# Optimization experiments

Hardware: AMD Instinct MI355X
Metric: run time of the kernel (lower is better)

## Reference

```python
import jax, jax.numpy as jnp
import numpy as np

D_MODEL, N_HEADS, D_FF = 768, 12, 3072
B, S = 2, 2048
EPS = 1e-6

def _ln(x, alpha, bias):
    # Matches torch: std with Bessel correction (unbiased), scalar alpha/bias
    mean = x.mean(axis=-1, keepdims=True)
    std = jnp.std(x, axis=-1, keepdims=True, ddof=1)
    return alpha * (x - mean) / (std + EPS) + bias

def setup_inputs() -> dict:
    key = jax.random.key(0)
    ks = jax.random.split(key, 12)
    def w(k, shp):
        return jax.random.normal(k, shp, dtype=jnp.float32) * 0.02
    inp = {
        "x": jax.random.normal(ks[0], (B, S, D_MODEL), dtype=jnp.float32),
        "mask": jnp.ones((B, 1, 1, S), dtype=jnp.int32),
        "wq": w(ks[1], (D_MODEL, D_MODEL)), "bq": jnp.zeros((D_MODEL,), jnp.float32),
        "wk": w(ks[2], (D_MODEL, D_MODEL)), "bk": jnp.zeros((D_MODEL,), jnp.float32),
        "wv": w(ks[3], (D_MODEL, D_MODEL)), "bv": jnp.zeros((D_MODEL,), jnp.float32),
        "wo": w(ks[4], (D_MODEL, D_MODEL)), "bo": jnp.zeros((D_MODEL,), jnp.float32),
        "w1": w(ks[5], (D_MODEL, D_FF)), "b1": jnp.zeros((D_FF,), jnp.float32),
        "w2": w(ks[6], (D_FF, D_MODEL)), "b2": jnp.zeros((D_MODEL,), jnp.float32),
        "ln1_a": jnp.ones((1,), jnp.float32), "ln1_b": jnp.zeros((1,), jnp.float32),
        "ln2_a": jnp.ones((1,), jnp.float32), "ln2_b": jnp.zeros((1,), jnp.float32),
    }
    return inp

def reference(x, mask, wq, bq, wk, bk, wv, bv, wo, bo, w1, b1, w2, b2,
              ln1_a, ln1_b, ln2_a, ln2_b):
    d_k = D_MODEL // N_HEADS
    # --- residual 1: pre-LN self-attention ---
    h = _ln(x, ln1_a, ln1_b)
    q = (h @ wq + bq).reshape(B, S, N_HEADS, d_k).transpose(0, 2, 1, 3)
    k = (h @ wk + bk).reshape(B, S, N_HEADS, d_k).transpose(0, 2, 1, 3)
    v = (h @ wv + bv).reshape(B, S, N_HEADS, d_k).transpose(0, 2, 1, 3)
    scores = jnp.einsum('bhqd,bhkd->bhqk', q, k) / jnp.sqrt(jnp.float32(d_k))
    scores = jnp.where(mask == 0, jnp.float32(-1e9), scores)
    attn = jax.nn.softmax(scores, axis=-1)            # [B,H,S,S] materialized, as in source
    ctx = jnp.einsum('bhqk,bhkd->bhqd', attn, v)
    ctx = ctx.transpose(0, 2, 1, 3).reshape(B, S, D_MODEL)
    x = x + (ctx @ wo + bo)
    # --- residual 2: pre-LN FFN ---
    h = _ln(x, ln2_a, ln2_b)
    ffn = jax.nn.relu(h @ w1 + b1) @ w2 + b2
    return x + ffn
```

## Files before the change

### kernel.cpp

```cpp
#include <hip/hip_runtime.h>
#include <math.h>

#define DM    768
#define NH    12
#define DKH   64
#define DFF   3072
#define BATCH 2
#define SLEN  2048
#define MTOT  4096
#define LNEPS 1e-6f
#define QSCALE 0.18033688011112042f

typedef unsigned short u16;
typedef __attribute__((ext_vector_type(8))) short bf16x8;
typedef __attribute__((ext_vector_type(4))) float f32x4;
typedef __attribute__((ext_vector_type(4))) unsigned short us4;

__device__ __forceinline__ u16 f2bf(float f) {
    union { float f; unsigned int u; } v; v.f = f;
    unsigned int r = v.u + 0x7FFFu + ((v.u >> 16) & 1u);
    return (u16)(r >> 16);
}

__device__ __forceinline__ unsigned pk2bf_t(float lo, float hi) {
    union { float f; unsigned u; } a, b;
    a.f = lo; b.f = hi;
    return __builtin_amdgcn_perm(b.u, a.u, 0x07060302u);
}

__device__ __forceinline__ void gld16(const void* g, void* lds) {
    __builtin_amdgcn_global_load_lds(
        (const __attribute__((address_space(1))) unsigned int*)(unsigned long long)g,
        (__attribute__((address_space(3))) unsigned int*)(unsigned int)(unsigned long long)lds,
        16, 0, 0);
}

__device__ __forceinline__ void xcd_map(int id, int Nb, int& bm, int& bn) {
    int xcd = id & 7, loc = id >> 3;
    bn = loc % Nb;
    bm = (loc / Nb) * 8 + xcd;
}

__device__ __forceinline__ void ln_body(const float* __restrict__ x,
                                        u16* __restrict__ out,
                                        const float* __restrict__ alpha_p,
                                        const float* __restrict__ beta_p,
                                        const float* __restrict__ b2,
                                        float* __restrict__ out2, int row) {
    const float* xr = x + (size_t)row * DM;
    int t = threadIdx.x;
    float v0 = xr[t], v1 = xr[t + 256], v2 = xr[t + 512];
    float s = v0 + v1 + v2;
    #pragma unroll
    for (int off = 32; off > 0; off >>= 1) s += __shfl_down(s, off);
    __shared__ float red[4], red2[4];
    int wv = t >> 6, ln = t & 63;
    if (ln == 0) red[wv] = s;
    __syncthreads();
    float mean = (red[0] + red[1] + red[2] + red[3]) * (1.0f / 768.0f);
    float d0 = v0 - mean, d1 = v1 - mean, d2 = v2 - mean;
    float sq = d0 * d0 + d1 * d1 + d2 * d2;
    #pragma unroll
    for (int off = 32; off > 0; off >>= 1) sq += __shfl_down(sq, off);
    if (ln == 0) red2[wv] = sq;
    __syncthreads();
    float var = (red2[0] + red2[1] + red2[2] + red2[3]) * (1.0f / 767.0f);
    float scale = alpha_p[0] / (sqrtf(var) + LNEPS);
    float bias = beta_p[0];
    u16* orow = out + (size_t)row * DM;
    orow[t]       = f2bf(d0 * scale + bias);
    orow[t + 256] = f2bf(d1 * scale + bias);
    orow[t + 512] = f2bf(d2 * scale + bias);
    if (out2) {
        float* o2 = out2 + (size_t)row * DM;
        o2[t]       = v0 + b2[t];
        o2[t + 256] = v1 + b2[t + 256];
        o2[t + 512] = v2 + b2[t + 512];
    }
}

__global__ __launch_bounds__(256) void ln_kernel(const float* __restrict__ x,
                                                 u16* __restrict__ out,
                                                 const float* __restrict__ alpha_p,
                                                 const float* __restrict__ beta_p,
                                                 const float* __restrict__ b2,
                                                 float* __restrict__ out2) {
    ln_body(x, out, alpha_p, beta_p, b2, out2, blockIdx.x);
}

__device__ __forceinline__ void wcast_body(const float* __restrict__ src,
                                           u16* __restrict__ dst,
                                           int R, int C, int bx, int by) {
    __shared__ float tile[32][33];
    int t = threadIdx.x, tx = t & 31, ty = t >> 5;
    int r0 = by * 32, c0 = bx * 32;
    #pragma unroll
    for (int p = 0; p < 4; p++)
        tile[ty + p * 8][tx] = src[(size_t)(r0 + ty + p * 8) * C + c0 + tx];
    __syncthreads();
    #pragma unroll
    for (int p = 0; p < 4; p++)
        dst[(size_t)(c0 + ty + p * 8) * R + r0 + tx] = f2bf(tile[tx][ty + p * 8]);
}

__global__ __launch_bounds__(256) void prep_kernel(
        const float* __restrict__ x, u16* __restrict__ h,
        const float* __restrict__ ln1a, const float* __restrict__ ln1b,
        const float* __restrict__ wq, const float* __restrict__ wk,
        const float* __restrict__ wv, const float* __restrict__ wo,
        const float* __restrict__ w1, const float* __restrict__ w2,
        u16* __restrict__ wqT, u16* __restrict__ wkT, u16* __restrict__ wvT,
        u16* __restrict__ woT, u16* __restrict__ w1T, u16* __restrict__ w2T) {
    int bid = blockIdx.x;
    if (bid < MTOT) {
        ln_body(x, h, ln1a, ln1b, nullptr, nullptr, bid);
        return;
    }
    bid -= MTOT;
    const float* src; u16* dst; int R, C, bx, by;
    if (bid < 2304) {
        int j = bid / 576, tix = bid % 576;
        R = 768; C = 768; bx = tix % 24; by = tix / 24;
        src = (j == 0) ? wq : (j == 1) ? wk : (j == 2) ? wv : wo;
        dst = (j == 0) ? wqT : (j == 1) ? wkT : (j == 2) ? wvT : woT;
    } else if (bid < 4608) {
        int tix = bid - 2304;
        R = 768; C = 3072; bx = tix % 96; by = tix / 96;
        src = w1; dst = w1T;
    } else {
        int tix = bid - 4608;
        R = 3072; C = 768; bx = tix % 24; by = tix / 24;
        src = w2; dst = w2T;
    }
    wcast_body(src, dst, R, C, bx, by);
}

template<int EPI>
__device__ __forceinline__ void gemm128_core(const u16* __restrict__ A,
                                             const u16* __restrict__ Wt,
                                             const float* __restrict__ bias,
                                             const float* __restrict__ resid,
                                             void* __restrict__ Cout,
                                             int M, int N, int Kstride, int Kloop,
                                             float scale, int bm, int bn) {
    __shared__ __align__(16) u16 As[2][128 * 32];
    __shared__ __align__(16) u16 Bs[2][128 * 32];
    int t = threadIdx.x;
    int ln = t & 63, w = t >> 6;
    int wm = w >> 1, wn = w & 1;
    int quad = ln >> 4, col = ln & 15;
    int m0 = bm * 128, n0 = bn * 128;

    f32x4 acc[4][4];
    const f32x4 zero = {0.f, 0.f, 0.f, 0.f};
    #pragma unroll
    for (int i = 0; i < 4; i++)
        #pragma unroll
        for (int j = 0; j < 4; j++) acc[i][j] = zero;

    int st_ch = (((ln & 3) ^ ((ln >> 3) & 3))) * 8;
    const u16* Ag = A  + (size_t)(m0 + 32 * w + (ln >> 2)) * Kstride + st_ch;
    const u16* Bg = Wt + (size_t)(n0 + 32 * w + (ln >> 2)) * Kstride + st_ch;

    gld16(Ag,                As[0] + w * 1024);
    gld16(Ag + 16 * Kstride, As[0] + w * 1024 + 512);
    gld16(Bg,                Bs[0] + w * 1024);
    gld16(Bg + 16 * Kstride, Bs[0] + w * 1024 + 512);
    __syncthreads();

    int rch = (quad ^ ((col >> 1) & 3)) * 8;

    for (int k0 = 0; k0 < Kloop; k0 += 32) {
        int cur = (k0 >> 5) & 1, nxt = cur ^ 1;
        if (k0 + 32 < Kloop) {
            gld16(Ag + k0 + 32,                As[nxt] + w * 1024);
            gld16(Ag + k0 + 32 + 16 * Kstride, As[nxt] + w * 1024 + 512);
            gld16(Bg + k0 + 32,                Bs[nxt] + w * 1024);
            gld16(Bg + k0 + 32 + 16 * Kstride, Bs[nxt] + w * 1024 + 512);
        }
        bf16x8 af[4], bfr[4];
        #pragma unroll
        for (int i = 0; i < 4; i++)
            af[i] = *(const bf16x8*)&As[cur][(wm * 64 + i * 16 + col) * 32 + rch];
        #pragma unroll
        for (int j = 0; j < 4; j++)
            bfr[j] = *(const bf16x8*)&Bs[cur][(wn * 64 + j * 16 + col) * 32 + rch];
        #pragma unroll
        for (int i = 0; i < 4; i++)
            #pragma unroll
            for (int j = 0; j < 4; j++)
                acc[i][j] = __builtin_amdgcn_mfma_f32_16x16x32_bf16(af[i], bfr[j], acc[i][j], 0, 0, 0);
        __syncthreads();
    }

    #pragma unroll
    for (int i = 0; i < 4; i++) {
        int mb = m0 + wm * 64 + i * 16 + quad * 4;
        #pragma unroll
        for (int j = 0; j < 4; j++) {
            int n = n0 + wn * 64 + j * 16 + col;
            if (EPI == 0 || EPI == 1) {
                float bs = bias[n];
                u16* Cb = (u16*)Cout;
                #pragma unroll
                for (int r = 0; r < 4; r++) {
                    float f = (acc[i][j][r] + bs) * ((EPI == 0) ? scale : 1.0f);
                    if (EPI == 1) f = fmaxf(f, 0.f);
                    Cb[(size_t)(mb + r) * N + n] = f2bf(f);
                }
            } else if (EPI == 2) {
                float bs = bias[n];
                float* Cf = (float*)Cout;
                #pragma unroll
                for (int r = 0; r < 4; r++)
                    Cf[(size_t)(mb + r) * N + n] =
                        acc[i][j][r] + bs + resid[(size_t)(mb + r) * N + n];
            } else if (EPI == 3) {
                float bs = bias[n];
                u16* Cb = (u16*)Cout;
                us4 pk;
                #pragma unroll
                for (int r = 0; r < 4; r++) pk[r] = f2bf(acc[i][j][r] + bs);
                *(us4*)&Cb[(size_t)n * M + mb] = pk;
            } else {
                float* Cf = (float*)Cout;
                #pragma unroll
                for (int r = 0; r < 4; r++)
                    atomicAdd(&Cf[(size_t)(mb + r) * N + n], acc[i][j][r]);
            }
        }
    }
}

template<int EPI>
__global__ __launch_bounds__(256) void gemm_kernel(const u16* __restrict__ A,
                                                   const u16* __restrict__ Wt,
                                                   const float* __restrict__ bias,
                                                   const float* __restrict__ resid,
                                                   void* __restrict__ C,
                                                   int M, int N, int Kstride, int Kloop,
                                                   float scale, int Nb) {
    const u16* Az = A  + (size_t)blockIdx.z * Kloop;
    const u16* Wz = Wt + (size_t)blockIdx.z * Kloop;
    int bm, bn;
    xcd_map(blockIdx.x, Nb, bm, bn);
    gemm128_core<EPI>(Az, Wz, bias, resid, C, M, N, Kstride, Kloop, scale, bm, bn);
}

__global__ __launch_bounds__(256) void qkv_kernel(const u16* __restrict__ h,
        const u16* __restrict__ wqT, const u16* __restrict__ wkT, const u16* __restrict__ wvT,
        const float* __restrict__ bq, const float* __restrict__ bk, const float* __restrict__ bv,
        u16* __restrict__ q, u16* __restrict__ k, u16* __restrict__ vT) {
    int z = blockIdx.z;
    int bm, bn;
    xcd_map(blockIdx.x, 6, bm, bn);
    if (z == 0)      gemm128_core<0>(h, wqT, bq, nullptr, q,  MTOT, DM, DM, DM, QSCALE, bm, bn);
    else if (z == 1) gemm128_core<0>(h, wkT, bk, nullptr, k,  MTOT, DM, DM, DM, 1.0f,   bm, bn);
    else             gemm128_core<3>(h, wvT, bv, nullptr, vT, MTOT, DM, DM, DM, 1.0f,   bm, bn);
}

template<int EPI>
__global__ __launch_bounds__(256) void gemm64_kernel(const u16* __restrict__ A,
                                                     const u16* __restrict__ Wt,
                                                     const float* __restrict__ bias,
                                                     const float* __restrict__ resid,
                                                     void* __restrict__ Cout,
                                                     int M, int N, int Kstride, int Kloop,
                                                     int Nb) {
    __shared__ __align__(16) u16 As[2][64 * 32];
    __shared__ __align__(16) u16 Bs[2][64 * 32];
    int t = threadIdx.x, ln = t & 63, w = t >> 6;
    int wm = w >> 1, wn = w & 1;
    int quad = ln >> 4, col = ln & 15;
    int bm, bn;
    xcd_map(blockIdx.x, Nb, bm, bn);
    int m0 = bm * 64, n0 = bn * 64;

    f32x4 acc[2][2];
    const f32x4 zero = {0.f, 0.f, 0.f, 0.f};
    #pragma unroll
    for (int i = 0; i < 2; i++)
        #pragma unroll
        for (int j = 0; j < 2; j++) acc[i][j] = zero;

    int st_ch = (((ln & 3) ^ ((ln >> 3) & 3))) * 8;
    const u16* Ag = A  + (size_t)(m0 + 16 * w + (ln >> 2)) * Kstride + st_ch;
    const u16* Bg = Wt + (size_t)(n0 + 16 * w + (ln >> 2)) * Kstride + st_ch;
    gld16(Ag, As[0] + w * 512);
    gld16(Bg, Bs[0] + w * 512);
    __syncthreads();

    int rch = (quad ^ ((col >> 1) & 3)) * 8;

    for (int k0 = 0; k0 < Kloop; k0 += 32) {
        int cur = (k0 >> 5) & 1, nxt = cur ^ 1;
        if (k0 + 32 < Kloop) {
            gld16(Ag + k0 + 32, As[nxt] + w * 512);
            gld16(Bg + k0 + 32, Bs[nxt] + w * 512);
        }
        bf16x8 af[2], bfr[2];
        #pragma unroll
        for (int i = 0; i < 2; i++)
            af[i] = *(const bf16x8*)&As[cur][(wm * 32 + i * 16 + col) * 32 + rch];
        #pragma unroll
        for (int j = 0; j < 2; j++)
            bfr[j] = *(const bf16x8*)&Bs[cur][(wn * 32 + j * 16 + col) * 32 + rch];
        #pragma unroll
        for (int i = 0; i < 2; i++)
            #pragma unroll
            for (int j = 0; j < 2; j++)
                acc[i][j] = __builtin_amdgcn_mfma_f32_16x16x32_bf16(af[i], bfr[j], acc[i][j], 0, 0, 0);
        __syncthreads();
    }

    #pragma unroll
    for (int i = 0; i < 2; i++) {
        int mb = m0 + wm * 32 + i * 16 + quad * 4;
        #pragma unroll
        for (int j = 0; j < 2; j++) {
            int n = n0 + wn * 32 + j * 16 + col;
            float bs = bias[n];
            float* Cf = (float*)Cout;
            #pragma unroll
            for (int r = 0; r < 4; r++)
                Cf[(size_t)(mb + r) * N + n] =
                    acc[i][j][r] + bs + resid[(size_t)(mb + r) * N + n];
        }
    }
}

__global__ __launch_bounds__(256) void attn_kernel(const u16* __restrict__ qg,
                                                   const u16* __restrict__ kg,
                                                   const u16* __restrict__ vTg,
                                                   const int* __restrict__ mask,
                                                   u16* __restrict__ ctx) {
    __shared__ __align__(16) u16 Qs[64 * 64];
    __shared__ __align__(16) u16 KV[4][64 * 64];
    __shared__ __align__(16) u16 Ps[4][32 * 40];
    __shared__ __align__(16) float Msf[2][64];
    __shared__ float Lp[64];
    int t = threadIdx.x, ln = t & 63, w = t >> 6;
    int quad = ln >> 4, col = ln & 15;
    int qh = w >> 1, kh = w & 1;
    int bh = blockIdx.x, qb = blockIdx.y;
    int b = bh / NH, h = bh - b * NH;
    int q0 = qb * 64;
    size_t qkbase = ((size_t)b * SLEN) * DM + h * DKH;
    size_t vbase  = ((size_t)h * DKH) * MTOT + (size_t)b * SLEN;

    int sw_st = (((ln & 7) ^ (ln >> 3)) * 8);

    {
        const u16* g0 = qg + qkbase + (size_t)(q0 + 16 * w + (ln >> 3)) * DM + sw_st;
        gld16(g0,          Qs + w * 1024);
        gld16(g0 + 8 * DM, Qs + w * 1024 + 512);
        const u16* kg0 = kg + qkbase + (size_t)(16 * w + (ln >> 3)) * DM + sw_st;
        gld16(kg0,          KV[0] + w * 1024);
        gld16(kg0 + 8 * DM, KV[0] + w * 1024 + 512);
        const u16* vg0 = vTg + vbase + (size_t)(16 * w + (ln >> 3)) * MTOT + sw_st;
        gld16(vg0,            KV[2] + w * 1024);
        gld16(vg0 + 8 * MTOT, KV[2] + w * 1024 + 512);
        if (t < 64) Msf[0][t] = mask[b * SLEN + t] ? 0.f : -1e9f;
    }
    __syncthreads();

    bf16x8 bqf[2][2];
    #pragma unroll
    for (int qgi = 0; qgi < 2; qgi++) {
        int rq = qh * 32 + qgi * 16 + col;
        int cq = ((quad ^ (rq & 7)) * 8);
        bqf[qgi][0] = *(const bf16x8*)&Qs[rq * 64 + cq];
        bqf[qgi][1] = *(const bf16x8*)&Qs[rq * 64 + (cq ^ 32)];
    }

    bf16x8 vones;
    #pragma unroll
    for (int i = 0; i < 8; i++) vones[i] = (short)0x3F80;

    const u16* kpn = kg + qkbase + (size_t)(64 + 16 * w + (ln >> 3)) * DM + sw_st;
    const u16* vpn = vTg + vbase + (size_t)(16 * w + (ln >> 3)) * MTOT + 64 + sw_st;
    const int* mpn = mask + b * SLEN + 64 + t;

    f32x4 Ov[2][4], Lv[2];
    const f32x4 zero = {0.f, 0.f, 0.f, 0.f};
    #pragma unroll
    for (int qgi = 0; qgi < 2; qgi++) {
        Lv[qgi] = zero;
        #pragma unroll
        for (int dg = 0; dg < 4; dg++) Ov[qgi][dg] = zero;
    }
    u16* Psw = &Ps[w][0];

    #define ATTN_TILE(cur)                                                              \
    {                                                                                   \
        bf16x8 ak[2][2];                                                                \
        _Pragma("unroll")                                                               \
        for (int kgi = 0; kgi < 2; kgi++) {                                             \
            int rk = kh * 32 + kgi * 16 + col;                                          \
            int ck = ((quad ^ (rk & 7)) * 8);                                           \
            ak[kgi][0] = *(const bf16x8*)&KV[cur][rk * 64 + ck];                        \
            ak[kgi][1] = *(const bf16x8*)&KV[cur][rk * 64 + (ck ^ 32)];                 \
        }                                                                               \
        _Pragma("unroll")                                                               \
        for (int kgi = 0; kgi < 2; kgi++) {                                             \
            f32x4 bias4 = *(const f32x4*)&Msf[cur][kh * 32 + kgi * 16 + quad * 4];      \
            _Pragma("unroll")                                                           \
            for (int qgi = 0; qgi < 2; qgi++) {                                         \
                f32x4 S = __builtin_amdgcn_mfma_f32_16x16x32_bf16(ak[kgi][0], bqf[qgi][0], bias4, 0, 0, 0); \
                S       = __builtin_amdgcn_mfma_f32_16x16x32_bf16(ak[kgi][1], bqf[qgi][1], S,     0, 0, 0); \
                float p0 = exp2f(S[0]), p1 = exp2f(S[1]);                               \
                float p2 = exp2f(S[2]), p3 = exp2f(S[3]);                               \
                uint2 pk;                                                               \
                pk.x = pk2bf_t(p0, p1);                                                 \
                pk.y = pk2bf_t(p2, p3);                                                 \
                *(uint2*)&Psw[(qgi * 16 + col) * 40 + kgi * 16 + quad * 4] = pk;        \
            }                                                                           \
        }                                                                               \
        bf16x8 ap[2];                                                                   \
        _Pragma("unroll")                                                               \
        for (int qgi = 0; qgi < 2; qgi++) {                                             \
            ap[qgi] = *(const bf16x8*)&Psw[(qgi * 16 + col) * 40 + quad * 8];           \
            Lv[qgi] = __builtin_amdgcn_mfma_f32_16x16x32_bf16(ap[qgi], vones, Lv[qgi], 0, 0, 0); \
        }                                                                               \
        _Pragma("unroll")                                                               \
        for (int dg = 0; dg < 4; dg++) {                                                \
            int rv = dg * 16 + col;                                                     \
            int cv = (((kh * 4 + quad) ^ (rv & 7)) * 8);                                \
            bf16x8 bv = *(const bf16x8*)&KV[2 + cur][rv * 64 + cv];                     \
            Ov[0][dg] = __builtin_amdgcn_mfma_f32_16x16x32_bf16(ap[0], bv, Ov[0][dg], 0, 0, 0); \
            Ov[1][dg] = __builtin_amdgcn_mfma_f32_16x16x32_bf16(ap[1], bv, Ov[1][dg], 0, 0, 0); \
        }                                                                               \
        __syncthreads();                                                                \
    }

    for (int it = 0; it < SLEN / 64 - 1; it++) {
        int cur = it & 1, nxt = cur ^ 1;
        gld16(kpn,            KV[nxt] + w * 1024);
        gld16(kpn + 8 * DM,   KV[nxt] + w * 1024 + 512);
        gld16(vpn,            KV[2 + nxt] + w * 1024);
        gld16(vpn + 8 * MTOT, KV[2 + nxt] + w * 1024 + 512);
        if (t < 64) Msf[nxt][t] = *mpn ? 0.f : -1e9f;
        kpn += 64 * DM; vpn += 64; mpn += 64;
        ATTN_TILE(cur)
    }
    ATTN_TILE((SLEN / 64 - 1) & 1)
    #undef ATTN_TILE

    float* Osh = (float*)&KV[0][0];
    if (kh == 1) {
        #pragma unroll
        for (int qgi = 0; qgi < 2; qgi++) {
            #pragma unroll
            for (int dg = 0; dg < 4; dg++)
                *(f32x4*)&Osh[(qh * 64 + dg * 16 + col) * 36 + qgi * 16 + quad * 4] = Ov[qgi][dg];
            if (col == 0) {
                #pragma unroll
                for (int r = 0; r < 4; r++)
                    Lp[qh * 32 + qgi * 16 + quad * 4 + r] = Lv[qgi][r];
            }
        }
    }
    __syncthreads();
    if (kh == 0) {
        #pragma unroll
        for (int qgi = 0; qgi < 2; qgi++) {
            float linv[4];
            #pragma unroll
            for (int r = 0; r < 4; r++) {
                int ql = qh * 32 + qgi * 16 + quad * 4 + r;
                linv[r] = 1.0f / (Lv[qgi][r] + Lp[ql]);
            }
            #pragma unroll
            for (int dg = 0; dg < 4; dg++) {
                f32x4 oo = *(const f32x4*)&Osh[(qh * 64 + dg * 16 + col) * 36 + qgi * 16 + quad * 4];
                #pragma unroll
                for (int r = 0; r < 4; r++) {
                    int qrow = q0 + qh * 32 + qgi * 16 + quad * 4 + r;
                    ctx[qkbase + (size_t)qrow * DM + dg * 16 + col] =
                        f2bf((Ov[qgi][dg][r] + oo[r]) * linv[r]);
                }
            }
        }
    }
}

extern "C" void kernel_launch(void* const* d_in, const int* in_sizes, int n_in,
                              void* d_out, int out_size, void* d_ws, size_t ws_size,
                              hipStream_t stream) {
    const float* x    = (const float*)d_in[0];
    const int*   mask = (const int*)d_in[1];
    const float* wq   = (const float*)d_in[2];
    const float* bq   = (const float*)d_in[3];
    const float* wk   = (const float*)d_in[4];
    const float* bk   = (const float*)d_in[5];
    const float* wv   = (const float*)d_in[6];
    const float* bv   = (const float*)d_in[7];
    const float* wo   = (const float*)d_in[8];
    const float* bo   = (const float*)d_in[9];
    const float* w1   = (const float*)d_in[10];
    const float* b1   = (const float*)d_in[11];
    const float* w2   = (const float*)d_in[12];
    const float* b2   = (const float*)d_in[13];
    const float* ln1a = (const float*)d_in[14];
    const float* ln1b = (const float*)d_in[15];
    const float* ln2a = (const float*)d_in[16];
    const float* ln2b = (const float*)d_in[17];
    float* out = (float*)d_out;

    char* w8 = (char*)d_ws;
    u16*   ffn = (u16*)(w8 + 0);
    u16*   q   = (u16*)(w8 + 0);
    u16*   kb  = (u16*)(w8 + 6291456);
    u16*   vT  = (u16*)(w8 + 12582912);
    u16*   ctx = (u16*)(w8 + 18874368);
    u16*   h   = (u16*)(w8 + 25165824);
    float* x1  = (float*)(w8 + 31457280);
    u16*   wqT = (u16*)(w8 + 44040192);
    u16*   wkT = (u16*)(w8 + 45219840);
    u16*   wvT = (u16*)(w8 + 46399488);
    u16*   woT = (u16*)(w8 + 47579136);
    u16*   w1T = (u16*)(w8 + 48758784);
    u16*   w2T = (u16*)(w8 + 53477376);

    prep_kernel<<<MTOT + 6912, 256, 0, stream>>>(x, h, ln1a, ln1b,
                                                 wq, wk, wv, wo, w1, w2,
                                                 wqT, wkT, wvT, woT, w1T, w2T);
    qkv_kernel<<<dim3(192, 1, 3), 256, 0, stream>>>(h, wqT, wkT, wvT, bq, bk, bv, q, kb, vT);
    attn_kernel<<<dim3(BATCH * NH, SLEN / 64), 256, 0, stream>>>(q, kb, vT, mask, ctx);
    gemm64_kernel<2><<<768, 256, 0, stream>>>(ctx, woT, bo, x, (void*)x1,
                                              MTOT, DM, DM, DM, 12);
    ln_kernel<<<MTOT, 256, 0, stream>>>(x1, h, ln2a, ln2b, b2, out);
    gemm_kernel<1><<<768, 256, 0, stream>>>(h, w1T, b1, nullptr, (void*)ffn,
                                            MTOT, DFF, DM, DM, 1.0f, 24);
    gemm_kernel<5><<<dim3(192, 1, 2), 256, 0, stream>>>(ffn, w2T, nullptr, nullptr, (void*)out,
                                                        MTOT, DM, DFF, DFF / 2, 1.0f, 6);
}
```

Before: 287.0 us.

## Shrink attention LDS footprint by aliasing Q/P buffers and moving mask to registers

Merges the separate shared buffers into one 40KB array: the Q tile region is reused for per-wave P staging after Q fragments are loaded into registers, and the padded P layout (stride 40) is replaced by an XOR-swizzled stride-32 layout. The per-tile mask bias is no longer staged through LDS; each lane loads its int4 mask values directly from global memory one tile ahead and converts them in registers. The aim is lower LDS usage per block, which allows higher occupancy and removes LDS traffic for the mask. In exchange it adds an extra barrier, a little register pressure, and hand-computed offsets for the epilogue buffers.

```diff
diff --git a/kernel.cpp b/kernel.cpp
--- a/kernel.cpp
+++ b/kernel.cpp
@@ -334,11 +334,9 @@
                                                    const u16* __restrict__ vTg,
                                                    const int* __restrict__ mask,
                                                    u16* __restrict__ ctx) {
-    __shared__ __align__(16) u16 Qs[64 * 64];
-    __shared__ __align__(16) u16 KV[4][64 * 64];
-    __shared__ __align__(16) u16 Ps[4][32 * 40];
-    __shared__ __align__(16) float Msf[2][64];
-    __shared__ float Lp[64];
+    __shared__ __align__(16) u16 SMEM[20480];
+    u16* KVb = SMEM;
+    u16* QsPs = SMEM + 16384;
     int t = threadIdx.x, ln = t & 63, w = t >> 6;
     int quad = ln >> 4, col = ln & 15;
     int qh = w >> 1, kh = w & 1;
@@ -352,16 +350,19 @@
 
     {
         const u16* g0 = qg + qkbase + (size_t)(q0 + 16 * w + (ln >> 3)) * DM + sw_st;
-        gld16(g0,          Qs + w * 1024);
-        gld16(g0 + 8 * DM, Qs + w * 1024 + 512);
+        gld16(g0,          QsPs + w * 1024);
+        gld16(g0 + 8 * DM, QsPs + w * 1024 + 512);
         const u16* kg0 = kg + qkbase + (size_t)(16 * w + (ln >> 3)) * DM + sw_st;
-        gld16(kg0,          KV[0] + w * 1024);
-        gld16(kg0 + 8 * DM, KV[0] + w * 1024 + 512);
+        gld16(kg0,          KVb + w * 1024);
+        gld16(kg0 + 8 * DM, KVb + w * 1024 + 512);
         const u16* vg0 = vTg + vbase + (size_t)(16 * w + (ln >> 3)) * MTOT + sw_st;
-        gld16(vg0,            KV[2] + w * 1024);
-        gld16(vg0 + 8 * MTOT, KV[2] + w * 1024 + 512);
-        if (t < 64) Msf[0][t] = mask[b * SLEN + t] ? 0.f : -1e9f;
-    }
+        gld16(vg0,            KVb + 2 * 4096 + w * 1024);
+        gld16(vg0 + 8 * MTOT, KVb + 2 * 4096 + w * 1024 + 512);
+    }
+    const int* mbase = mask + b * SLEN + kh * 32 + quad * 4;
+    int4 mreg[2];
+    mreg[0] = *(const int4*)(mbase);
+    mreg[1] = *(const int4*)(mbase + 16);
     __syncthreads();
 
     bf16x8 bqf[2][2];
@@ -369,9 +370,10 @@
     for (int qgi = 0; qgi < 2; qgi++) {
         int rq = qh * 32 + qgi * 16 + col;
         int cq = ((quad ^ (rq & 7)) * 8);
-        bqf[qgi][0] = *(const bf16x8*)&Qs[rq * 64 + cq];
-        bqf[qgi][1] = *(const bf16x8*)&Qs[rq * 64 + (cq ^ 32)];
-    }
+        bqf[qgi][0] = *(const bf16x8*)&QsPs[rq * 64 + cq];
+        bqf[qgi][1] = *(const bf16x8*)&QsPs[rq * 64 + (cq ^ 32)];
+    }
+    __syncthreads();
 
     bf16x8 vones;
     #pragma unroll
@@ -379,7 +381,6 @@
 
     const u16* kpn = kg + qkbase + (size_t)(64 + 16 * w + (ln >> 3)) * DM + sw_st;
     const u16* vpn = vTg + vbase + (size_t)(16 * w + (ln >> 3)) * MTOT + 64 + sw_st;
-    const int* mpn = mask + b * SLEN + 64 + t;
 
     f32x4 Ov[2][4], Lv[2];
     const f32x4 zero = {0.f, 0.f, 0.f, 0.f};
@@ -389,7 +390,8 @@
         #pragma unroll
         for (int dg = 0; dg < 4; dg++) Ov[qgi][dg] = zero;
     }
-    u16* Psw = &Ps[w][0];
+    u16* Psw = QsPs + w * 1024;
+    int ps_s = (col >> 1) & 3;
 
     #define ATTN_TILE(cur)                                                              \
     {                                                                                   \
@@ -398,12 +400,16 @@
         for (int kgi = 0; kgi < 2; kgi++) {                                             \
             int rk = kh * 32 + kgi * 16 + col;                                          \
             int ck = ((quad ^ (rk & 7)) * 8);                                           \
-            ak[kgi][0] = *(const bf16x8*)&KV[cur][rk * 64 + ck];                        \
-            ak[kgi][1] = *(const bf16x8*)&KV[cur][rk * 64 + (ck ^ 32)];                 \
+            ak[kgi][0] = *(const bf16x8*)&KVb[(cur) * 4096 + rk * 64 + ck];             \
+            ak[kgi][1] = *(const bf16x8*)&KVb[(cur) * 4096 + rk * 64 + (ck ^ 32)];      \
         }                                                                               \
         _Pragma("unroll")                                                               \
         for (int kgi = 0; kgi < 2; kgi++) {                                             \
-            f32x4 bias4 = *(const f32x4*)&Msf[cur][kh * 32 + kgi * 16 + quad * 4];      \
+            f32x4 bias4;                                                                \
+            bias4[0] = mreg[kgi].x ? 0.f : -1e9f;                                       \
+            bias4[1] = mreg[kgi].y ? 0.f : -1e9f;                                       \
+            bias4[2] = mreg[kgi].z ? 0.f : -1e9f;                                       \
+            bias4[3] = mreg[kgi].w ? 0.f : -1e9f;                                       \
             _Pragma("unroll")                                                           \
             for (int qgi = 0; qgi < 2; qgi++) {                                         \
                 f32x4 S = __builtin_amdgcn_mfma_f32_16x16x32_bf16(ak[kgi][0], bqf[qgi][0], bias4, 0, 0, 0); \
@@ -413,20 +419,21 @@
                 uint2 pk;                                                               \
                 pk.x = pk2bf_t(p0, p1);                                                 \
                 pk.y = pk2bf_t(p2, p3);                                                 \
-                *(uint2*)&Psw[(qgi * 16 + col) * 40 + kgi * 16 + quad * 4] = pk;        \
+                *(uint2*)&Psw[(qgi * 16 + col) * 32 +                                   \
+                              (((kgi * 2 + (quad >> 1)) ^ ps_s) * 8) + (quad & 1) * 4] = pk; \
             }                                                                           \
         }                                                                               \
         bf16x8 ap[2];                                                                   \
         _Pragma("unroll")                                                               \
         for (int qgi = 0; qgi < 2; qgi++) {                                             \
-            ap[qgi] = *(const bf16x8*)&Psw[(qgi * 16 + col) * 40 + quad * 8];           \
+            ap[qgi] = *(const bf16x8*)&Psw[(qgi * 16 + col) * 32 + ((quad ^ ps_s) * 8)]; \
             Lv[qgi] = __builtin_amdgcn_mfma_f32_16x16x32_bf16(ap[qgi], vones, Lv[qgi], 0, 0, 0); \
         }                                                                               \
         _Pragma("unroll")                                                               \
         for (int dg = 0; dg < 4; dg++) {                                                \
             int rv = dg * 16 + col;                                                     \
             int cv = (((kh * 4 + quad) ^ (rv & 7)) * 8);                                \
-            bf16x8 bv = *(const bf16x8*)&KV[2 + cur][rv * 64 + cv];                     \
+            bf16x8 bv = *(const bf16x8*)&KVb[(2 + (cur)) * 4096 + rv * 64 + cv];        \
             Ov[0][dg] = __builtin_amdgcn_mfma_f32_16x16x32_bf16(ap[0], bv, Ov[0][dg], 0, 0, 0); \
             Ov[1][dg] = __builtin_amdgcn_mfma_f32_16x16x32_bf16(ap[1], bv, Ov[1][dg], 0, 0, 0); \
         }                                                                               \
@@ -435,18 +442,22 @@
 
     for (int it = 0; it < SLEN / 64 - 1; it++) {
         int cur = it & 1, nxt = cur ^ 1;
-        gld16(kpn,            KV[nxt] + w * 1024);
-        gld16(kpn + 8 * DM,   KV[nxt] + w * 1024 + 512);
-        gld16(vpn,            KV[2 + nxt] + w * 1024);
-        gld16(vpn + 8 * MTOT, KV[2 + nxt] + w * 1024 + 512);
-        if (t < 64) Msf[nxt][t] = *mpn ? 0.f : -1e9f;
-        kpn += 64 * DM; vpn += 64; mpn += 64;
+        gld16(kpn,            KVb + nxt * 4096 + w * 1024);
+        gld16(kpn + 8 * DM,   KVb + nxt * 4096 + w * 1024 + 512);
+        gld16(vpn,            KVb + (2 + nxt) * 4096 + w * 1024);
+        gld16(vpn + 8 * MTOT, KVb + (2 + nxt) * 4096 + w * 1024 + 512);
+        int4 mnxt0 = *(const int4*)(mbase + (it + 1) * 64);
+        int4 mnxt1 = *(const int4*)(mbase + (it + 1) * 64 + 16);
+        kpn += 64 * DM; vpn += 64;
         ATTN_TILE(cur)
+        mreg[0] = mnxt0;
+        mreg[1] = mnxt1;
     }
     ATTN_TILE((SLEN / 64 - 1) & 1)
     #undef ATTN_TILE
 
-    float* Osh = (float*)&KV[0][0];
+    float* Osh = (float*)SMEM;
+    float* Lp  = (float*)&SMEM[9300];
     if (kh == 1) {
         #pragma unroll
         for (int qgi = 0; qgi < 2; qgi++) {
```

Result: no change. 291.0 us (+1.4%).
